# Performance work log

Hardware: AMD Instinct MI355X
Metric: run time of the kernel (lower is better)

## Reference

```python
import jax, jax.numpy as jnp
import numpy as np

TOP_K = 2
EPS = float(np.finfo(np.float64).eps)  # combine() clamps zeros to np.finfo(float).eps


def setup_inputs() -> dict:
    key = jax.random.key(0)
    ks = jax.random.split(key, 6)
    B, D, H, O, E = 2048, 1024, 2048, 512, 8
    return {
        "x": jax.random.normal(ks[0], (B, D), dtype=jnp.float32),
        "w_gate": jax.random.normal(ks[1], (D, E), dtype=jnp.float32) * 0.02,
        "fc1_w": jax.random.normal(ks[2], (E, D, H), dtype=jnp.float32) * 0.02,
        "fc1_b": jax.random.normal(ks[3], (E, H), dtype=jnp.float32) * 0.02,
        "fc2_w": jax.random.normal(ks[4], (E, H, O), dtype=jnp.float32) * 0.02,
        "fc2_b": jax.random.normal(ks[5], (E, O), dtype=jnp.float32) * 0.02,
    }


def _gates(x, w_gate):
    # Noisy top-k gating in eval mode (no noise): clean logits -> top-k -> softmax over top-k -> scatter.
    logits = x @ w_gate                              # [B, E]
    top_logits, top_idx = jax.lax.top_k(logits, TOP_K)  # [B, K]
    top_gates = jax.nn.softmax(top_logits, axis=-1)      # 'softmax' gating over selected experts
    B = x.shape[0]
    gates = jnp.zeros(logits.shape, logits.dtype)
    gates = gates.at[jnp.arange(B)[:, None], top_idx].set(top_gates)
    return gates                                      # [B, E], zero for non-selected experts


def reference(x, w_gate, fc1_w, fc1_b, fc2_w, fc2_b):
    gates = _gates(x, w_gate)                         # [B, E]
    # Dense-equivalent of SparseDispatcher: non-selected experts have gate 0,
    # so weighting by gates reproduces dispatch/expert/combine exactly.
    h = jax.nn.gelu(jnp.einsum('bd,edh->ebh', x, fc1_w) + fc1_b[:, None, :],
                    approximate=False)                # [E, B, H]
    logp = jax.nn.log_softmax(jnp.einsum('ebh,eho->ebo', h, fc2_w) + fc2_b[:, None, :],
                              axis=-1)                # [E, B, O] (MLP ends with LogSoftmax)
    # combine: sum_e gates[b,e] * exp(logp_e[b]), clamp zeros to eps, then log
    combined = jnp.einsum('ebo,be->bo', jnp.exp(logp), gates)  # [B, O]
    combined = jnp.where(combined == 0, jnp.asarray(EPS, combined.dtype), combined)
    return jnp.log(combined)
```

## Files before the change

kernel.cpp:

```cpp
#include <hip/hip_runtime.h>
#include <stdint.h>

#define Bn 2048
#define Dn 1024
#define Hn 2048
#define On 512
#define En 8

typedef float f32x4 __attribute__((ext_vector_type(4)));
typedef unsigned char u8;

__device__ __forceinline__ void gload16(const void* g, void* l) {
  __builtin_amdgcn_global_load_lds((const uint32_t*)g, (uint32_t*)l, 16, 0, 0);
}

__device__ __forceinline__ u8 f2fp8(float v) {
  int w = __builtin_amdgcn_cvt_pk_fp8_f32(v, v, 0, false);
  return (u8)(w & 0xff);
}

__global__ void init_kernel(int* counts, int* cursors) {
  int t = threadIdx.x;
  if (t < En) { counts[t] = 0; cursors[t] = 0; }
}

#define NB_G (Bn / 8)
#define NB_T1 ((Dn / 64) * (Hn / 64) * En)
#define NB_T2 ((Hn / 64) * (On / 64) * En)
#define WSCALE 64.0f

__device__ __forceinline__ void tcast_f8_64(const float* __restrict__ inp,
                                            u8* __restrict__ outp,
                                            int R, int C, int r0, int c0, uint32_t* L) {
  int t = threadIdx.x;
  int cc4 = (t & 15) * 4;
  int rg = t >> 4;
  uint32_t wds[4] = {0, 0, 0, 0};
#pragma unroll
  for (int i = 0; i < 4; i++) {
    float4 v = *(const float4*)&inp[(size_t)(r0 + rg * 4 + i) * C + c0 + cc4];
    wds[0] |= (uint32_t)f2fp8(v.x * WSCALE) << (8 * i);
    wds[1] |= (uint32_t)f2fp8(v.y * WSCALE) << (8 * i);
    wds[2] |= (uint32_t)f2fp8(v.z * WSCALE) << (8 * i);
    wds[3] |= (uint32_t)f2fp8(v.w * WSCALE) << (8 * i);
  }
#pragma unroll
  for (int j = 0; j < 4; j++) L[(cc4 + j) * 17 + rg] = wds[j];
  __syncthreads();
  int c = t >> 2, q = t & 3;
  int4 o;
#pragma unroll
  for (int i = 0; i < 4; i++) ((int*)&o)[i] = (int)L[c * 17 + q * 4 + i];
  *(int4*)&outp[(size_t)(c0 + c) * R + r0 + q * 16] = o;
}

__global__ __launch_bounds__(256) void prep_kernel(
    const float* __restrict__ x, const float* __restrict__ wg,
    const float* __restrict__ fc1w, const float* __restrict__ fc2w,
    u8* __restrict__ x_f8, u8* __restrict__ w1t8, u8* __restrict__ w2t8,
    int* __restrict__ top_idx, float* __restrict__ gates, int* __restrict__ counts) {
  __shared__ __align__(16) uint32_t smem[64 * 17];
  __shared__ int lcnt[En];
  int bid = blockIdx.x;
  int t = threadIdx.x;

  if (bid < NB_G) {
    if (t < En) lcnt[t] = 0;
    __syncthreads();
    int w = t >> 6, lane = t & 63;
#pragma unroll
    for (int r = 0; r < 2; r++) {
      int b = bid * 8 + w * 2 + r;
      const float* xr = x + (size_t)b * Dn;
      u8* xo = x_f8 + (size_t)b * Dn;
      float acc[En];
#pragma unroll
      for (int e = 0; e < En; e++) acc[e] = 0.f;
#pragma unroll
      for (int j = 0; j < 16; j++) {
        int d = lane + j * 64;
        float xv = xr[d];
        xo[d] = f2fp8(xv);
        float4 wa = *(const float4*)(wg + (size_t)d * En);
        float4 wb = *(const float4*)(wg + (size_t)d * En + 4);
        acc[0] += xv * wa.x; acc[1] += xv * wa.y;
        acc[2] += xv * wa.z; acc[3] += xv * wa.w;
        acc[4] += xv * wb.x; acc[5] += xv * wb.y;
        acc[6] += xv * wb.z; acc[7] += xv * wb.w;
      }
#pragma unroll
      for (int off = 32; off; off >>= 1) {
#pragma unroll
        for (int e = 0; e < En; e++) acc[e] += __shfl_down(acc[e], off);
      }
      if (lane == 0) {
        float best = -1e30f, second = -1e30f; int bi = 0, si = 0;
#pragma unroll
        for (int e = 0; e < En; e++) {
          float l = acc[e];
          if (l > best) { second = best; si = bi; best = l; bi = e; }
          else if (l > second) { second = l; si = e; }
        }
        float e1 = expf(second - best);
        float inv = 1.f / (1.f + e1);
        top_idx[2 * b] = bi; top_idx[2 * b + 1] = si;
        gates[2 * b] = inv;  gates[2 * b + 1] = e1 * inv;
        atomicAdd(&lcnt[bi], 1);
        atomicAdd(&lcnt[si], 1);
      }
    }
    __syncthreads();
    if (t < En) {
      int c = lcnt[t];
      if (c) atomicAdd(&counts[t], c);
    }
  } else if (bid < NB_G + NB_T1) {
    int idx = bid - NB_G;
    constexpr int TPE = (Dn / 64) * (Hn / 64);
    int z = idx / TPE, rem = idx % TPE;
    int r0 = (rem / (Hn / 64)) * 64, c0 = (rem % (Hn / 64)) * 64;
    tcast_f8_64(fc1w + (size_t)z * Dn * Hn, w1t8 + (size_t)z * Dn * Hn, Dn, Hn, r0, c0, smem);
  } else {
    int idx = bid - NB_G - NB_T1;
    constexpr int TPE = (Hn / 64) * (On / 64);
    int z = idx / TPE, rem = idx % TPE;
    int r0 = (rem / (On / 64)) * 64, c0 = (rem % (On / 64)) * 64;
    tcast_f8_64(fc2w + (size_t)z * Hn * On, w2t8 + (size_t)z * Hn * On, Hn, On, r0, c0, smem);
  }
}

__global__ void assign_kernel(const int* __restrict__ top_idx, const int* __restrict__ counts,
                              int* cursors, int* __restrict__ s2r, int* __restrict__ r2s) {
  int b = blockIdx.x * 256 + threadIdx.x;
  if (b >= Bn) return;
  int offs[En];
  int s = 0;
#pragma unroll
  for (int e = 0; e < En; e++) { offs[e] = s; s += counts[e]; }
#pragma unroll
  for (int k = 0; k < 2; k++) {
    int e = top_idx[2 * b + k];
    int pos = atomicAdd(&cursors[e], 1);
    int slot = offs[e] + pos;
    s2r[slot] = b;
    r2s[2 * b + k] = slot;
  }
}

template <bool FC1, int N, int K, int SPLITK>
__global__ __launch_bounds__(256, 8) void fp8_gemm_kernel(
    const u8* __restrict__ A, const u8* __restrict__ WT,
    const float* __restrict__ bias, const int* __restrict__ counts,
    const int* __restrict__ s2r,
    u8* __restrict__ outH8, float* __restrict__ outL, float* __restrict__ outL2) {
  constexpr int NBL = N / 64;
  constexpr int KS = K / SPLITK;
  constexpr int NT = KS / 64;
  int e = blockIdx.z;
  int cnt = counts[e];
  int rb = blockIdx.y;
  if (rb * 64 >= cnt) return;
  int base = 0;
#pragma unroll
  for (int i = 0; i < En; i++) base += (i < e) ? counts[i] : 0;
  int ks = blockIdx.x / NBL;
  int nb = (blockIdx.x % NBL) * 64;
  int k0 = ks * KS;
  __shared__ __align__(16) u8 As[64 * 64];
  __shared__ __align__(16) u8 Bs[64 * 64];
  int t = threadIdx.x;
  int lane = t & 63, w = t >> 6;
  int wr = w >> 1, wc = w & 1;

  int srow = t >> 2;
  int sslot = (t & 3) ^ ((srow >> 1) & 3);
  int scol = sslot * 16;

  int lr = rb * 64 + srow;
  int lrc = lr < cnt ? lr : cnt - 1;
  const u8* aptr = A + (size_t)(FC1 ? s2r[base + lrc] : (base + lrc)) * K + k0 + scol;
  const u8* bptr = WT + ((size_t)e * N + nb + srow) * K + k0 + scol;

  f32x4 zero = {0.f, 0.f, 0.f, 0.f};
  f32x4 acc[2][2];
#pragma unroll
  for (int m = 0; m < 2; m++)
#pragma unroll
    for (int n = 0; n < 2; n++) acc[m][n] = zero;

  int a_r = wr * 32 + (lane & 15);
  int b_r = wc * 32 + (lane & 15);
  int rkey = ((lane & 15) >> 1) & 3;
  int slb = (lane >> 4) >> 1;
  int half = ((lane >> 4) & 1) * 8;

  for (int kt = 0; kt < NT; kt++) {
    gload16(aptr + kt * 64, &As[t * 16]);
    gload16(bptr + kt * 64, &Bs[t * 16]);
    __syncthreads();
#pragma unroll
    for (int kk = 0; kk < 2; kk++) {
      long af[2], bfr[2];
#pragma unroll
      for (int m = 0; m < 2; m++)
        af[m] = *(const long*)(As + (a_r + m * 16) * 64 +
                               (((kk * 2 + slb) ^ rkey) << 4) + half);
#pragma unroll
      for (int n = 0; n < 2; n++)
        bfr[n] = *(const long*)(Bs + (b_r + n * 16) * 64 +
                                (((kk * 2 + slb) ^ rkey) << 4) + half);
#pragma unroll
      for (int m = 0; m < 2; m++)
#pragma unroll
        for (int n = 0; n < 2; n++)
          acc[m][n] = __builtin_amdgcn_mfma_f32_16x16x32_fp8_fp8(af[m], bfr[n], acc[m][n], 0, 0, 0);
    }
    __syncthreads();
  }

  const float INV = 1.0f / WSCALE;
  float* dst = (SPLITK > 1 && ks > 0) ? outL2 : outL;
  int lr0 = rb * 64 + wr * 32;
#pragma unroll
  for (int m = 0; m < 2; m++) {
#pragma unroll
    for (int i = 0; i < 4; i++) {
      int orow = lr0 + m * 16 + (lane >> 4) * 4 + i;
      if (orow < cnt) {
        int slot = base + orow;
#pragma unroll
        for (int n = 0; n < 2; n++) {
          int col = nb + wc * 32 + n * 16 + (lane & 15);
          if (FC1) {
            float v = acc[m][n][i] * INV + bias[e * N + col];
            float g = 0.5f * v * (1.0f + erff(v * 0.70710678118654752f));
            outH8[(size_t)slot * N + col] = f2fp8(g);
          } else {
            float v = acc[m][n][i] * INV + (ks == 0 ? bias[e * N + col] : 0.f);
            dst[(size_t)slot * N + col] = v;
          }
        }
      }
    }
  }
}

__device__ __forceinline__ float blk_reduce(float v, bool ismax) {
  __shared__ float sbuf[4];
  int lane = threadIdx.x & 63, w = threadIdx.x >> 6;
#pragma unroll
  for (int off = 32; off; off >>= 1) {
    float o = __shfl_down(v, off);
    v = ismax ? fmaxf(v, o) : (v + o);
  }
  __syncthreads();
  if (lane == 0) sbuf[w] = v;
  __syncthreads();
  float r = sbuf[0];
#pragma unroll
  for (int i = 1; i < 4; i++) r = ismax ? fmaxf(r, sbuf[i]) : (r + sbuf[i]);
  return r;
}

__global__ void combine_kernel(const float* __restrict__ l2a, const float* __restrict__ l2b,
                               const int* __restrict__ r2s, const float* __restrict__ gates,
                               float* __restrict__ out) {
  int b = blockIdx.x, t = threadIdx.x;
  float c0 = 0.f, c1 = 0.f;
#pragma unroll
  for (int k = 0; k < 2; k++) {
    int slot = r2s[2 * b + k];
    float g = gates[2 * b + k];
    const float* lp0 = l2a + (size_t)slot * On;
    const float* lp1 = l2b + (size_t)slot * On;
    float v0 = lp0[t] + lp1[t];
    float v1 = lp0[t + 256] + lp1[t + 256];
    float m = blk_reduce(fmaxf(v0, v1), true);
    float s = blk_reduce(expf(v0 - m) + expf(v1 - m), false);
    float lse = m + logf(s);
    c0 += g * expf(v0 - lse);
    c1 += g * expf(v1 - lse);
  }
  const float EPSv = 2.220446049250313e-16f;
  out[(size_t)b * On + t] = logf(fmaxf(c0, EPSv));
  out[(size_t)b * On + t + 256] = logf(fmaxf(c1, EPSv));
}

extern "C" void kernel_launch(void* const* d_in, const int* in_sizes, int n_in,
                              void* d_out, int out_size, void* d_ws, size_t ws_size,
                              hipStream_t stream) {
  const float* x = (const float*)d_in[0];
  const float* wgate = (const float*)d_in[1];
  const float* fc1w = (const float*)d_in[2];
  const float* fc1b = (const float*)d_in[3];
  const float* fc2w = (const float*)d_in[4];
  const float* fc2b = (const float*)d_in[5];
  float* out = (float*)d_out;

  char* ws = (char*)d_ws;
  size_t o = 0;
  u8* x_f8     = (u8*)(ws + o);    o += (size_t)Bn * Dn;
  u8* w1t8     = (u8*)(ws + o);    o += (size_t)En * Hn * Dn;
  u8* w2t8     = (u8*)(ws + o);    o += (size_t)En * On * Hn;
  u8* hbuf8    = (u8*)(ws + o);    o += (size_t)2 * Bn * Hn;
  float* l2buf = (float*)(ws + o); o += (size_t)2 * Bn * On * 4;
  int* top_idx = (int*)(ws + o);   o += (size_t)Bn * 2 * 4;
  float* gates = (float*)(ws + o); o += (size_t)Bn * 2 * 4;
  int* r2s     = (int*)(ws + o);   o += (size_t)Bn * 2 * 4;
  int* s2r     = (int*)(ws + o);   o += (size_t)2 * Bn * 4;
  int* counts  = (int*)(ws + o);   o += 64;
  int* cursors = (int*)(ws + o);   o += 64;
  float* l2buf1 = (float*)w1t8;

  hipLaunchKernelGGL(init_kernel, dim3(1), dim3(64), 0, stream, counts, cursors);
  hipLaunchKernelGGL(prep_kernel, dim3(NB_G + NB_T1 + NB_T2), dim3(256), 0, stream,
                     x, wgate, fc1w, fc2w, x_f8, w1t8, w2t8, top_idx, gates, counts);
  hipLaunchKernelGGL(assign_kernel, dim3(Bn / 256), dim3(256), 0, stream,
                     top_idx, counts, cursors, s2r, r2s);
  hipLaunchKernelGGL((fp8_gemm_kernel<true, Hn, Dn, 1>), dim3(Hn / 64, 32, En), dim3(256),
                     0, stream, x_f8, w1t8, fc1b, counts, s2r, hbuf8,
                     (float*)nullptr, (float*)nullptr);
  hipLaunchKernelGGL((fp8_gemm_kernel<false, On, Hn, 2>), dim3((On / 64) * 2, 32, En), dim3(256),
                     0, stream, hbuf8, w2t8, fc2b, counts, s2r, (u8*)nullptr,
                     l2buf, l2buf1);
  hipLaunchKernelGGL(combine_kernel, dim3(Bn), dim3(256), 0, stream, l2buf, l2buf1, r2s, gates, out);
}
```

Before: 114.5 us.

## Raise FC2 split-K to four partials, pack fp8 conversion, memset counters

Result: no change. 114.6 us (+0.1%).

```diff
diff --git a/kernel.cpp b/kernel.cpp
--- a/kernel.cpp
+++ b/kernel.cpp
@@ -19,9 +19,10 @@
   return (u8)(w & 0xff);
 }
 
-__global__ void init_kernel(int* counts, int* cursors) {
-  int t = threadIdx.x;
-  if (t < En) { counts[t] = 0; cursors[t] = 0; }
+__device__ __forceinline__ uint32_t pk4_fp8(float a, float b, float c, float d) {
+  int w = __builtin_amdgcn_cvt_pk_fp8_f32(a, b, 0, false);
+  w = __builtin_amdgcn_cvt_pk_fp8_f32(c, d, w, true);
+  return (uint32_t)w;
 }
 
 #define NB_G (Bn / 8)
@@ -35,15 +36,15 @@
   int t = threadIdx.x;
   int cc4 = (t & 15) * 4;
   int rg = t >> 4;
-  uint32_t wds[4] = {0, 0, 0, 0};
-#pragma unroll
-  for (int i = 0; i < 4; i++) {
-    float4 v = *(const float4*)&inp[(size_t)(r0 + rg * 4 + i) * C + c0 + cc4];
-    wds[0] |= (uint32_t)f2fp8(v.x * WSCALE) << (8 * i);
-    wds[1] |= (uint32_t)f2fp8(v.y * WSCALE) << (8 * i);
-    wds[2] |= (uint32_t)f2fp8(v.z * WSCALE) << (8 * i);
-    wds[3] |= (uint32_t)f2fp8(v.w * WSCALE) << (8 * i);
-  }
+  float4 v0 = *(const float4*)&inp[(size_t)(r0 + rg * 4 + 0) * C + c0 + cc4];
+  float4 v1 = *(const float4*)&inp[(size_t)(r0 + rg * 4 + 1) * C + c0 + cc4];
+  float4 v2 = *(const float4*)&inp[(size_t)(r0 + rg * 4 + 2) * C + c0 + cc4];
+  float4 v3 = *(const float4*)&inp[(size_t)(r0 + rg * 4 + 3) * C + c0 + cc4];
+  uint32_t wds[4];
+  wds[0] = pk4_fp8(v0.x * WSCALE, v1.x * WSCALE, v2.x * WSCALE, v3.x * WSCALE);
+  wds[1] = pk4_fp8(v0.y * WSCALE, v1.y * WSCALE, v2.y * WSCALE, v3.y * WSCALE);
+  wds[2] = pk4_fp8(v0.z * WSCALE, v1.z * WSCALE, v2.z * WSCALE, v3.z * WSCALE);
+  wds[3] = pk4_fp8(v0.w * WSCALE, v1.w * WSCALE, v2.w * WSCALE, v3.w * WSCALE);
 #pragma unroll
   for (int j = 0; j < 4; j++) L[(cc4 + j) * 17 + rg] = wds[j];
   __syncthreads();
@@ -152,7 +153,7 @@
     const u8* __restrict__ A, const u8* __restrict__ WT,
     const float* __restrict__ bias, const int* __restrict__ counts,
     const int* __restrict__ s2r,
-    u8* __restrict__ outH8, float* __restrict__ outL, float* __restrict__ outL2) {
+    u8* __restrict__ outH8, float* __restrict__ outL, float* __restrict__ outLX) {
   constexpr int NBL = N / 64;
   constexpr int KS = K / SPLITK;
   constexpr int NT = KS / 64;
@@ -219,7 +220,7 @@
   }
 
   const float INV = 1.0f / WSCALE;
-  float* dst = (SPLITK > 1 && ks > 0) ? outL2 : outL;
+  float* dst = (SPLITK > 1 && ks > 0) ? (outLX + (size_t)(ks - 1) * (2 * Bn * On)) : outL;
   int lr0 = rb * 64 + wr * 32;
 #pragma unroll
   for (int m = 0; m < 2; m++) {
@@ -262,7 +263,7 @@
   return r;
 }
 
-__global__ void combine_kernel(const float* __restrict__ l2a, const float* __restrict__ l2b,
+__global__ void combine_kernel(const float* __restrict__ l2a, const float* __restrict__ l2x,
                                const int* __restrict__ r2s, const float* __restrict__ gates,
                                float* __restrict__ out) {
   int b = blockIdx.x, t = threadIdx.x;
@@ -272,9 +273,13 @@
     int slot = r2s[2 * b + k];
     float g = gates[2 * b + k];
     const float* lp0 = l2a + (size_t)slot * On;
-    const float* lp1 = l2b + (size_t)slot * On;
-    float v0 = lp0[t] + lp1[t];
-    float v1 = lp0[t + 256] + lp1[t + 256];
+    float v0 = lp0[t], v1 = lp0[t + 256];
+#pragma unroll
+    for (int p = 0; p < 3; p++) {
+      const float* lpp = l2x + (size_t)p * (2 * Bn * On) + (size_t)slot * On;
+      v0 += lpp[t];
+      v1 += lpp[t + 256];
+    }
     float m = blk_reduce(fmaxf(v0, v1), true);
     float s = blk_reduce(expf(v0 - m) + expf(v1 - m), false);
     float lse = m + logf(s);
@@ -299,20 +304,20 @@
 
   char* ws = (char*)d_ws;
   size_t o = 0;
-  u8* x_f8     = (u8*)(ws + o);    o += (size_t)Bn * Dn;
-  u8* w1t8     = (u8*)(ws + o);    o += (size_t)En * Hn * Dn;
-  u8* w2t8     = (u8*)(ws + o);    o += (size_t)En * On * Hn;
-  u8* hbuf8    = (u8*)(ws + o);    o += (size_t)2 * Bn * Hn;
-  float* l2buf = (float*)(ws + o); o += (size_t)2 * Bn * On * 4;
-  int* top_idx = (int*)(ws + o);   o += (size_t)Bn * 2 * 4;
-  float* gates = (float*)(ws + o); o += (size_t)Bn * 2 * 4;
-  int* r2s     = (int*)(ws + o);   o += (size_t)Bn * 2 * 4;
-  int* s2r     = (int*)(ws + o);   o += (size_t)2 * Bn * 4;
-  int* counts  = (int*)(ws + o);   o += 64;
-  int* cursors = (int*)(ws + o);   o += 64;
-  float* l2buf1 = (float*)w1t8;
-
-  hipLaunchKernelGGL(init_kernel, dim3(1), dim3(64), 0, stream, counts, cursors);
+  u8* x_f8      = (u8*)(ws + o);    o += (size_t)Bn * Dn;
+  u8* w1t8      = (u8*)(ws + o);    o += (size_t)En * Hn * Dn;
+  u8* w2t8      = (u8*)(ws + o);    o += (size_t)En * On * Hn;
+  u8* hbuf8     = (u8*)(ws + o);    o += (size_t)2 * Bn * Hn;
+  float* l2buf  = (float*)(ws + o); o += (size_t)2 * Bn * On * 4;
+  float* l2bufX = (float*)(ws + o); o += (size_t)3 * 2 * Bn * On * 4;
+  int* top_idx  = (int*)(ws + o);   o += (size_t)Bn * 2 * 4;
+  float* gates  = (float*)(ws + o); o += (size_t)Bn * 2 * 4;
+  int* r2s      = (int*)(ws + o);   o += (size_t)Bn * 2 * 4;
+  int* s2r      = (int*)(ws + o);   o += (size_t)2 * Bn * 4;
+  int* counts   = (int*)(ws + o);   o += 64;
+  int* cursors  = (int*)(ws + o);   o += 64;
+
+  hipMemsetAsync(counts, 0, 128, stream);
   hipLaunchKernelGGL(prep_kernel, dim3(NB_G + NB_T1 + NB_T2), dim3(256), 0, stream,
                      x, wgate, fc1w, fc2w, x_f8, w1t8, w2t8, top_idx, gates, counts);
   hipLaunchKernelGGL(assign_kernel, dim3(Bn / 256), dim3(256), 0, stream,
@@ -320,8 +325,8 @@
   hipLaunchKernelGGL((fp8_gemm_kernel<true, Hn, Dn, 1>), dim3(Hn / 64, 32, En), dim3(256),
                      0, stream, x_f8, w1t8, fc1b, counts, s2r, hbuf8,
                      (float*)nullptr, (float*)nullptr);
-  hipLaunchKernelGGL((fp8_gemm_kernel<false, On, Hn, 2>), dim3((On / 64) * 2, 32, En), dim3(256),
-                     0, stream, hbuf8, w2t8, fc2b, counts, s2r, (u8*)nullptr,
-                     l2buf, l2buf1);
-  hipLaunchKernelGGL(combine_kernel, dim3(Bn), dim3(256), 0, stream, l2buf, l2buf1, r2s, gates, out);
-}
+  hipLaunchKernelGGL((fp8_gemm_kernel<false, On, Hn, 4>), dim3((On / 64) * 4, 32, En),
+                     dim3(256), 0, stream, hbuf8, w2t8, fc2b, counts, s2r, (u8*)nullptr,
+                     l2buf, l2bufX);
+  hipLaunchKernelGGL(combine_kernel, dim3(Bn), dim3(256), 0, stream, l2buf, l2bufX, r2s, gates, out);
+}
```
